# Performance work log

Measured on AMD Instinct MI355X. Metric: run time of the kernel, lower is better.

## Reference

```python
import jax, jax.numpy as jnp
import numpy as np

B, S, DIN = 2, 2048, 1024
H = 16
DK = 1024   # dim_key_query_all
DV = 1024   # dim_value_all
DOUT = 1024
HEAD_SIZE = DK / H  # attention_head_size (float division in source)
LN_EPS = 1e-5


def setup_inputs() -> dict:
    key = jax.random.key(0)
    ks = jax.random.split(key, 12)
    s_in = 1.0 / np.sqrt(DIN)
    s_dv = 1.0 / np.sqrt(DV)
    return {
        "hidden_states": jax.random.normal(ks[0], (B, S, DIN), jnp.float32),
        "Wq": jax.random.uniform(ks[1], (DK, DIN), jnp.float32, -s_in, s_in),
        "Wk": jax.random.uniform(ks[2], (DK, DIN), jnp.float32, -s_in, s_in),
        "Wcb": jax.random.uniform(ks[3], (H, DIN), jnp.float32, -s_in, s_in),
        "Wv": jax.random.uniform(ks[4], (DV, DIN), jnp.float32, -s_in, s_in),
        "bv": jax.random.uniform(ks[5], (DV,), jnp.float32, -s_in, s_in),
        "mixing": 0.2 * jax.random.normal(ks[6], (H, DK), jnp.float32),
        "Wd": jax.random.uniform(ks[7], (DOUT, DV), jnp.float32, -s_dv, s_dv),
        "bd": jax.random.uniform(ks[8], (DOUT,), jnp.float32, -s_dv, s_dv),
        "gamma": jnp.ones((DV,), jnp.float32),
        "beta": jnp.zeros((DV,), jnp.float32),
    }


def reference(hidden_states, Wq, Wk, Wcb, Wv, bv, mixing, Wd, bd, gamma, beta):
    x = hidden_states  # [B, S, DIN]; self-attention: from == to
    q = jnp.einsum('bsd,kd->bsk', x, Wq)  # [B,S,DK]
    k = jnp.einsum('bsd,kd->bsk', x, Wk)  # [B,S,DK]
    # scores[b,h,i,j] = sum_c q[b,i,c]*mixing[h,c]*k[b,j,c]
    scores = jnp.einsum('bic,hc,bjc->bhij', q, mixing, k)
    cb = jnp.einsum('bjd,hd->bhj', x, Wcb)  # content bias [B,H,S]
    scores = scores + cb[:, :, None, :]
    scores = scores / jnp.sqrt(jnp.asarray(HEAD_SIZE, scores.dtype))
    probs = jax.nn.softmax(scores, axis=-1)  # dropout p=0.0 -> identity
    v = jnp.einsum('bsd,vd->bsv', x, Wv) + bv  # [B,S,DV]
    v = v.reshape(B, S, H, DV // H)
    ctx = jnp.einsum('bhij,bjhv->bihv', probs, v).reshape(B, S, DV)
    out = jnp.einsum('bsv,ov->bso', ctx, Wd) + bd
    res = x + out
    mu = jnp.mean(res, axis=-1, keepdims=True)
    var = jnp.var(res, axis=-1, keepdims=True)
    out = (res - mu) * jax.lax.rsqrt(var + LN_EPS) * gamma + beta
    return (out,)
```

## Files before the change

kernel.cpp:

```cpp
#include <hip/hip_runtime.h>
#include <cstddef>
#include <cstdint>

#define B_    2
#define S_    2048
#define DIN_  1024
#define H_    16
#define DK_   1024
#define DV_   1024
#define DH_   64
#define DOUT_ 1024
#define M_    (B_ * S_)

typedef __attribute__((ext_vector_type(8)))  short short8;
typedef __attribute__((ext_vector_type(4)))  float float4v;
typedef __attribute__((ext_vector_type(16))) float float16v;
typedef _Float16 half8v __attribute__((ext_vector_type(8)));

__device__ __forceinline__ float bf16s_to_f(short s) {
  union { unsigned int u; float f; } cv;
  cv.u = ((unsigned int)(unsigned short)s) << 16;
  return cv.f;
}
__device__ __forceinline__ short f_to_bf16s(float f) {
  union { float f; unsigned int u; } cv;
  cv.f = f;
  unsigned int u = cv.u + 0x7FFFu + ((cv.u >> 16) & 1u);
  return (short)(u >> 16);
}
__device__ __forceinline__ short f_to_f16s(float f) {
  union { _Float16 h; short s; } cv;
  cv.h = (_Float16)f;
  return cv.s;
}
__device__ __forceinline__ unsigned pkrtz_u32(float a, float b) {
  union { __fp16 __attribute__((ext_vector_type(2))) h2; unsigned u; } cv;
  cv.h2 = __builtin_amdgcn_cvt_pkrtz(a, b);
  return cv.u;
}
__device__ __forceinline__ void gll16(const void* g, void* l) {
  __builtin_amdgcn_global_load_lds(
      (const __attribute__((address_space(1))) unsigned int*)g,
      (__attribute__((address_space(3))) unsigned int*)l, 16, 0, 0);
}

__global__ __launch_bounds__(256) void cast_kernel(const float* __restrict__ in,
                                                   short* __restrict__ out, int n4) {
  int i = blockIdx.x * 256 + threadIdx.x;
  if (i >= n4) return;
  float4 v = ((const float4*)in)[i];
  union { ushort4 u; short s[4]; } o;
  o.s[0] = f_to_bf16s(v.x); o.s[1] = f_to_bf16s(v.y);
  o.s[2] = f_to_bf16s(v.z); o.s[3] = f_to_bf16s(v.w);
  ((ushort4*)out)[i] = o.u;
}

__global__ __launch_bounds__(256) void cb_kernel(const float* __restrict__ x,
                                                 const float* __restrict__ Wcb,
                                                 float* __restrict__ CBs) {
  __shared__ float xs[DIN_];
  const int row = blockIdx.x;
  const int tid = threadIdx.x;
  #pragma unroll
  for (int it = 0; it < 4; ++it)
    xs[tid + it * 256] = x[(size_t)row * DIN_ + tid + it * 256];
  __syncthreads();
  const int lane = tid & 63, w = tid >> 6;
  const float SC = 0.125f * 1.44269504088896f;
  #pragma unroll
  for (int hh = 0; hh < 4; ++hh) {
    const int hidx = w * 4 + hh;
    float p = 0.f;
    for (int c = lane; c < DIN_; c += 64)
      p += xs[c] * Wcb[(size_t)hidx * DIN_ + c];
    #pragma unroll
    for (int mk = 1; mk < 64; mk <<= 1) p += __shfl_xor(p, mk);
    if (lane == 0) {
      const int bb = row / S_, ss = row % S_;
      CBs[((size_t)bb * H_ + hidx) * S_ + ss] = p * SC;
    }
  }
}

__global__ __launch_bounds__(256, 2) void gemm_qkv(
    const short* __restrict__ A, const short* __restrict__ Wqb,
    const short* __restrict__ Wkb, const short* __restrict__ Wvb,
    const float* __restrict__ bv, short* __restrict__ Qf,
    short* __restrict__ Kf, short* __restrict__ Vtf) {
  const int KD = 1024;
  __shared__ short As[64][136];
  __shared__ short Bs[64][136];
  const int tid  = threadIdx.x;
  const int lane = tid & 63;
  const int w    = tid >> 6;
  const int quad = lane >> 4;
  const int l16  = lane & 15;
  const int sel  = blockIdx.x >> 4;
  const int n0   = (blockIdx.x & 15) * 64;
  const int m0   = blockIdx.y * 64;
  const short* Bw = sel == 0 ? Wqb : (sel == 1 ? Wkb : Wvb);
  const int wm   = (w >> 1) * 32;
  const int wn   = (w & 1) * 32;
  const int srow = tid >> 2;
  const int sseg = (tid & 3) * 32;

  const float4v zero = {0.f, 0.f, 0.f, 0.f};
  float4v acc[2][2];
  acc[0][0] = zero; acc[0][1] = zero; acc[1][0] = zero; acc[1][1] = zero;

  for (int k0 = 0; k0 < KD; k0 += 128) {
    short8 ar[4], br[4];
    #pragma unroll
    for (int c = 0; c < 4; ++c) {
      ar[c] = *(const short8*)(A  + (size_t)(m0 + srow) * KD + k0 + sseg + c * 8);
      br[c] = *(const short8*)(Bw + (size_t)(n0 + srow) * KD + k0 + sseg + c * 8);
    }
    __syncthreads();
    #pragma unroll
    for (int c = 0; c < 4; ++c) {
      *(short8*)&As[srow][sseg + c * 8] = ar[c];
      *(short8*)&Bs[srow][sseg + c * 8] = br[c];
    }
    __syncthreads();
    #pragma unroll
    for (int ks = 0; ks < 4; ++ks) {
      short8 af0 = *(short8*)&As[wm + l16][ks * 32 + quad * 8];
      short8 af1 = *(short8*)&As[wm + 16 + l16][ks * 32 + quad * 8];
      short8 bg0 = *(short8*)&Bs[wn + l16][ks * 32 + quad * 8];
      short8 bg1 = *(short8*)&Bs[wn + 16 + l16][ks * 32 + quad * 8];
      acc[0][0] = __builtin_amdgcn_mfma_f32_16x16x32_bf16(af0, bg0, acc[0][0], 0, 0, 0);
      acc[0][1] = __builtin_amdgcn_mfma_f32_16x16x32_bf16(af0, bg1, acc[0][1], 0, 0, 0);
      acc[1][0] = __builtin_amdgcn_mfma_f32_16x16x32_bf16(af1, bg0, acc[1][0], 0, 0, 0);
      acc[1][1] = __builtin_amdgcn_mfma_f32_16x16x32_bf16(af1, bg1, acc[1][1], 0, 0, 0);
    }
  }

  #pragma unroll
  for (int mt = 0; mt < 2; ++mt)
    #pragma unroll
    for (int nt = 0; nt < 2; ++nt)
      #pragma unroll
      for (int r = 0; r < 4; ++r) {
        int row = m0 + wm + mt * 16 + quad * 4 + r;
        int col = n0 + wn + nt * 16 + l16;
        float v = acc[mt][nt][r];
        if (sel == 2) {
          v += bv[col];
          int bb = row >> 11, ss = row & 2047;
          Vtf[((size_t)bb * DV_ + col) * S_ + ss] = f_to_f16s(v);
        } else {
          short* o = sel == 0 ? Qf : Kf;
          o[(size_t)row * 1024 + col] = f_to_f16s(v);
        }
      }
}

__global__ __launch_bounds__(256, 2) void gemm_out(
    const short* __restrict__ A, const short* __restrict__ Bw,
    const float* __restrict__ bias, const float* __restrict__ resid,
    float* __restrict__ outf) {
  const int KD = 1024, ND = 1024;
  __shared__ short As[64][136];
  __shared__ short Bs[64][136];
  const int tid  = threadIdx.x;
  const int lane = tid & 63;
  const int w    = tid >> 6;
  const int quad = lane >> 4;
  const int l16  = lane & 15;
  const int m0   = blockIdx.y * 64;
  const int n0   = blockIdx.x * 64;
  const int wm   = (w >> 1) * 32;
  const int wn   = (w & 1) * 32;
  const int srow = tid >> 2;
  const int sseg = (tid & 3) * 32;

  const float4v zero = {0.f, 0.f, 0.f, 0.f};
  float4v acc[2][2];
  acc[0][0] = zero; acc[0][1] = zero; acc[1][0] = zero; acc[1][1] = zero;

  for (int k0 = 0; k0 < KD; k0 += 128) {
    short8 ar[4], br[4];
    #pragma unroll
    for (int c = 0; c < 4; ++c) {
      ar[c] = *(const short8*)(A  + (size_t)(m0 + srow) * KD + k0 + sseg + c * 8);
      br[c] = *(const short8*)(Bw + (size_t)(n0 + srow) * KD + k0 + sseg + c * 8);
    }
    __syncthreads();
    #pragma unroll
    for (int c = 0; c < 4; ++c) {
      *(short8*)&As[srow][sseg + c * 8] = ar[c];
      *(short8*)&Bs[srow][sseg + c * 8] = br[c];
    }
    __syncthreads();
    #pragma unroll
    for (int ks = 0; ks < 4; ++ks) {
      short8 af0 = *(short8*)&As[wm + l16][ks * 32 + quad * 8];
      short8 af1 = *(short8*)&As[wm + 16 + l16][ks * 32 + quad * 8];
      short8 bg0 = *(short8*)&Bs[wn + l16][ks * 32 + quad * 8];
      short8 bg1 = *(short8*)&Bs[wn + 16 + l16][ks * 32 + quad * 8];
      acc[0][0] = __builtin_amdgcn_mfma_f32_16x16x32_bf16(af0, bg0, acc[0][0], 0, 0, 0);
      acc[0][1] = __builtin_amdgcn_mfma_f32_16x16x32_bf16(af0, bg1, acc[0][1], 0, 0, 0);
      acc[1][0] = __builtin_amdgcn_mfma_f32_16x16x32_bf16(af1, bg0, acc[1][0], 0, 0, 0);
      acc[1][1] = __builtin_amdgcn_mfma_f32_16x16x32_bf16(af1, bg1, acc[1][1], 0, 0, 0);
    }
  }

  #pragma unroll
  for (int mt = 0; mt < 2; ++mt)
    #pragma unroll
    for (int nt = 0; nt < 2; ++nt)
      #pragma unroll
      for (int r = 0; r < 4; ++r) {
        int row = m0 + wm + mt * 16 + quad * 4 + r;
        int col = n0 + wn + nt * 16 + l16;
        outf[(size_t)row * ND + col] =
            acc[mt][nt][r] + bias[col] + resid[(size_t)row * ND + col];
      }
}

__global__ __launch_bounds__(256, 2) void attn_kernel(
    const short* __restrict__ Qf, const short* __restrict__ Kf,
    const short* __restrict__ Vtf, const float* __restrict__ mixing,
    const float* __restrict__ CBs, short* __restrict__ ctxb) {
  __shared__ __align__(16) short Kbuf[2][128 * 64];
  __shared__ __align__(16) short Vt[64][136];
  __shared__ __align__(16) short mix_s[DK_];
  __shared__ float cb_s[128];

  const int tid  = threadIdx.x;
  const int lane = tid & 63;
  const int l32  = lane & 31;
  const int l1   = lane >> 5;
  const int w    = tid >> 6;

  const int F    = blockIdx.x;
  const int xcd  = F & 7, rest = F >> 3;
  const int b    = xcd >> 2;
  const int h    = (xcd & 3) * 4 + (rest & 3);
  const int i0   = (rest >> 2) * 128;

  const float SC = 0.125f * 1.44269504088896f;
  for (int c = tid; c < DK_; c += 256) {
    union { _Float16 h; short s; } cv;
    cv.h = (_Float16)(mixing[(size_t)h * DK_ + c] * SC);
    mix_s[c] = cv.s;
  }

  const int iq = i0 + w * 32 + l32;
  const short* qptr  = Qf + ((size_t)b * S_ + iq) * DK_;
  const short* kbase = Kf + (size_t)b * S_ * DK_;
  const short* vtb   = Vtf + ((size_t)b * DV_ + h * DH_) * S_;
  const float* cbp   = CBs + ((size_t)b * H_ + h) * S_;

  float16v accS[4], accO[2];
  #pragma unroll
  for (int g = 0; g < 2; ++g)
    #pragma unroll
    for (int r = 0; r < 16; ++r) accO[g][r] = 0.f;
  float m_run = -1e30f, l_run = 0.f;

  const int dr   = lane >> 3;
  const int lch  = (lane & 7) ^ dr;
  const int axor = l32 & 7;

  const int vrow = tid >> 2;
  const int vseg = (tid & 3) * 32;

  for (int j0 = 0; j0 < S_; j0 += 128) {
    short8 vreg[4];
    #pragma unroll
    for (int c = 0; c < 4; ++c)
      vreg[c] = *(const short8*)(vtb + (size_t)vrow * S_ + j0 + vseg + c * 8);
    float cbv = 0.f;
    if (tid < 128) cbv = cbp[j0 + tid];
    __syncthreads();
    #pragma unroll
    for (int c = 0; c < 4; ++c)
      *(short8*)&Vt[vrow][vseg + c * 8] = vreg[c];
    if (tid < 128) cb_s[tid] = cbv;

    #pragma unroll
    for (int cc = 0; cc < 4; ++cc) {
      const int n = w * 4 + cc, row = 8 * n + dr;
      gll16(kbase + (size_t)(j0 + row) * DK_ + lch * 8, &Kbuf[0][n * 512]);
    }
    half8v qcur[4];
    #pragma unroll
    for (int ks = 0; ks < 4; ++ks)
      qcur[ks] = *(const half8v*)(qptr + ks * 16 + l1 * 8);

    #pragma unroll
    for (int f = 0; f < 4; ++f)
      #pragma unroll
      for (int r = 0; r < 16; ++r) accS[f][r] = 0.f;

    #pragma unroll 2
    for (int c = 0; c < 16; ++c) {
      __syncthreads();
      if (c < 15) {
        const int cs = c + 1;
        #pragma unroll
        for (int cc = 0; cc < 4; ++cc) {
          const int n = w * 4 + cc, row = 8 * n + dr;
          gll16(kbase + (size_t)(j0 + row) * DK_ + cs * 64 + lch * 8,
                &Kbuf[cs & 1][n * 512]);
        }
      }
      half8v qnext[4];
      if (c < 15) {
        #pragma unroll
        for (int ks = 0; ks < 4; ++ks)
          qnext[ks] = *(const half8v*)(qptr + (c + 1) * 64 + ks * 16 + l1 * 8);
      }
      const short* kb = &Kbuf[c & 1][0];
      #pragma unroll
      for (int ks = 0; ks < 4; ++ks) {
        half8v mf = *(half8v*)&mix_s[c * 64 + ks * 16 + l1 * 8];
        half8v qm = qcur[ks] * mf;
        #pragma unroll
        for (int f = 0; f < 4; ++f) {
          const int r = f * 32 + l32;
          half8v af = *(const half8v*)&kb[r * 64 + ((2 * ks + l1) ^ axor) * 8];
          accS[f] = __builtin_amdgcn_mfma_f32_32x32x16_f16(af, qm, accS[f], 0, 0, 0);
        }
      }
      if (c < 15) {
        #pragma unroll
        for (int ks = 0; ks < 4; ++ks) qcur[ks] = qnext[ks];
      }
    }

    float tmax = -1e30f;
    #pragma unroll
    for (int f = 0; f < 4; ++f)
      #pragma unroll
      for (int q = 0; q < 4; ++q) {
        float4 cbq = *(float4*)&cb_s[f * 32 + q * 8 + l1 * 4];
        #pragma unroll
        for (int c = 0; c < 4; ++c) {
          accS[f][4 * q + c] += ((const float*)&cbq)[c];
          tmax = fmaxf(tmax, accS[f][4 * q + c]);
        }
      }
    tmax = fmaxf(tmax, __shfl_xor(tmax, 32));
    const float mnew = fmaxf(m_run, tmax);
    const float alpha = exp2f(m_run - mnew);
    float tsum = 0.f;
    #pragma unroll
    for (int f = 0; f < 4; ++f)
      #pragma unroll
      for (int r = 0; r < 16; ++r) {
        float pv = exp2f(accS[f][r] - mnew);
        accS[f][r] = pv;
        tsum += pv;
      }
    tsum += __shfl_xor(tsum, 32);
    l_run = l_run * alpha + tsum;
    m_run = mnew;
    #pragma unroll
    for (int g = 0; g < 2; ++g)
      #pragma unroll
      for (int r = 0; r < 16; ++r) accO[g][r] *= alpha;

    #pragma unroll
    for (int cpv = 0; cpv < 8; ++cpv) {
      const int t = cpv & 1, fp = cpv >> 1;
      float xo[4], yo[4], lo[4], hi[4];
      #pragma unroll
      for (int c = 0; c < 4; ++c) {
        xo[c] = __shfl_xor(accS[fp][8 * t + c], 32);
        yo[c] = __shfl_xor(accS[fp][8 * t + 4 + c], 32);
      }
      #pragma unroll
      for (int c = 0; c < 4; ++c) {
        lo[c] = l1 ? yo[c] : accS[fp][8 * t + c];
        hi[c] = l1 ? accS[fp][8 * t + 4 + c] : xo[c];
      }
      union { half8v v; unsigned u[4]; } pb;
      pb.u[0] = pkrtz_u32(lo[0], lo[1]);
      pb.u[1] = pkrtz_u32(lo[2], lo[3]);
      pb.u[2] = pkrtz_u32(hi[0], hi[1]);
      pb.u[3] = pkrtz_u32(hi[2], hi[3]);
      #pragma unroll
      for (int g = 0; g < 2; ++g) {
        half8v vf = *(half8v*)&Vt[g * 32 + l32][cpv * 16 + l1 * 8];
        accO[g] = __builtin_amdgcn_mfma_f32_32x32x16_f16(vf, pb.v, accO[g], 0, 0, 0);
      }
    }
  }

  const float rl = 1.0f / l_run;
  short* cbase = ctxb + ((size_t)b * S_ + iq) * DV_ + h * DH_;
  #pragma unroll
  for (int g = 0; g < 2; ++g)
    #pragma unroll
    for (int q = 0; q < 4; ++q) {
      const int dv = g * 32 + 8 * q + 4 * l1;
      union { ushort4 u4; short s[4]; } ov;
      #pragma unroll
      for (int r = 0; r < 4; ++r)
        ov.s[r] = f_to_bf16s(accO[g][4 * q + r] * rl);
      *(ushort4*)(cbase + dv) = ov.u4;
    }
}

__global__ __launch_bounds__(256) void ln_kernel(float* __restrict__ out,
                                                 const float* __restrict__ gamma,
                                                 const float* __restrict__ beta) {
  __shared__ float red[8];
  const int row = blockIdx.x;
  const int tid = threadIdx.x;
  float* p = out + (size_t)row * DOUT_;
  float4 v = ((const float4*)p)[tid];
  float s = v.x + v.y + v.z + v.w;
  #pragma unroll
  for (int mk = 1; mk < 64; mk <<= 1) s += __shfl_xor(s, mk);
  if ((tid & 63) == 0) red[tid >> 6] = s;
  __syncthreads();
  const float mean = (red[0] + red[1] + red[2] + red[3]) * (1.0f / 1024.0f);
  const float d0 = v.x - mean, d1 = v.y - mean, d2 = v.z - mean, d3 = v.w - mean;
  float sq = d0 * d0 + d1 * d1 + d2 * d2 + d3 * d3;
  #pragma unroll
  for (int mk = 1; mk < 64; mk <<= 1) sq += __shfl_xor(sq, mk);
  if ((tid & 63) == 0) red[4 + (tid >> 6)] = sq;
  __syncthreads();
  const float var = (red[4] + red[5] + red[6] + red[7]) * (1.0f / 1024.0f);
  const float rstd = rsqrtf(var + 1e-5f);
  float4 g = ((const float4*)gamma)[tid];
  float4 bt = ((const float4*)beta)[tid];
  float4 o;
  o.x = d0 * rstd * g.x + bt.x;
  o.y = d1 * rstd * g.y + bt.y;
  o.z = d2 * rstd * g.z + bt.z;
  o.w = d3 * rstd * g.w + bt.w;
  ((float4*)p)[tid] = o;
}

extern "C" void kernel_launch(void* const* d_in, const int* in_sizes, int n_in,
                              void* d_out, int out_size, void* d_ws, size_t ws_size,
                              hipStream_t stream) {
  (void)in_sizes; (void)n_in; (void)out_size; (void)ws_size;
  const float* x      = (const float*)d_in[0];
  const float* Wq     = (const float*)d_in[1];
  const float* Wk     = (const float*)d_in[2];
  const float* Wcb    = (const float*)d_in[3];
  const float* Wv     = (const float*)d_in[4];
  const float* bv     = (const float*)d_in[5];
  const float* mixing = (const float*)d_in[6];
  const float* Wd     = (const float*)d_in[7];
  const float* bd     = (const float*)d_in[8];
  const float* gamma  = (const float*)d_in[9];
  const float* beta   = (const float*)d_in[10];
  float* out = (float*)d_out;

  short* p = (short*)d_ws;
  short* xb   = p; p += (size_t)M_ * DIN_;
  short* Qf   = p; p += (size_t)M_ * DK_;
  short* Kf   = p; p += (size_t)M_ * DK_;
  short* Vtf  = p; p += (size_t)B_ * DV_ * S_;
  short* ctxb = p; p += (size_t)M_ * DV_;
  short* Wqb  = p; p += (size_t)DK_ * DIN_;
  short* Wkb  = p; p += (size_t)DK_ * DIN_;
  short* Wvb  = p; p += (size_t)DV_ * DIN_;
  short* Wdb  = p; p += (size_t)DOUT_ * DV_;
  float* CBs  = (float*)p;

  cast_kernel<<<dim3(M_ * DIN_ / 1024), 256, 0, stream>>>(x, xb, M_ * DIN_ / 4);
  cast_kernel<<<dim3(DK_ * DIN_ / 1024), 256, 0, stream>>>(Wq, Wqb, DK_ * DIN_ / 4);
  cast_kernel<<<dim3(DK_ * DIN_ / 1024), 256, 0, stream>>>(Wk, Wkb, DK_ * DIN_ / 4);
  cast_kernel<<<dim3(DV_ * DIN_ / 1024), 256, 0, stream>>>(Wv, Wvb, DV_ * DIN_ / 4);
  cast_kernel<<<dim3(DOUT_ * DV_ / 1024), 256, 0, stream>>>(Wd, Wdb, DOUT_ * DV_ / 4);
  cb_kernel<<<dim3(M_), 256, 0, stream>>>(x, Wcb, CBs);

  gemm_qkv<<<dim3(48, M_ / 64), 256, 0, stream>>>(xb, Wqb, Wkb, Wvb, bv, Qf, Kf, Vtf);

  attn_kernel<<<dim3(512), 256, 0, stream>>>(Qf, Kf, Vtf, mixing, CBs, ctxb);

  gemm_out<<<dim3(16, M_ / 64), 256, 0, stream>>>(ctxb, Wdb, bd, x, out);
  ln_kernel<<<dim3(M_), 256, 0, stream>>>(out, gamma, beta);
}
```

Before: 661.5 us.

## Widen K chunks and stream V/content-bias through shared double buffer in attention

The attention kernel now loads K in 128-wide column chunks, giving 8 chunks per key tile instead of 16, so it needs half as many barriers. V and the content bias are loaded asynchronously with global_load_lds into the same double buffer and overlap the last K chunk. The next tile's first K chunk is issued during softmax and PV. This replaces the synchronous register-staged V copy and the separate Vt and cb_s buffers, and uses an XOR swizzle over 16 columns. Shared memory rises to about 66KB, which may limit occupancy at two blocks per CU, and holding 16 Q registers raises register pressure.

```diff
diff --git a/kernel.cpp b/kernel.cpp
--- a/kernel.cpp
+++ b/kernel.cpp
@@ -42,6 +42,11 @@
   __builtin_amdgcn_global_load_lds(
       (const __attribute__((address_space(1))) unsigned int*)g,
       (__attribute__((address_space(3))) unsigned int*)l, 16, 0, 0);
+}
+__device__ __forceinline__ void gll4(const void* g, void* l) {
+  __builtin_amdgcn_global_load_lds(
+      (const __attribute__((address_space(1))) unsigned int*)g,
+      (__attribute__((address_space(3))) unsigned int*)l, 4, 0, 0);
 }
 
 __global__ __launch_bounds__(256) void cast_kernel(const float* __restrict__ in,
@@ -222,10 +227,8 @@
     const short* __restrict__ Qf, const short* __restrict__ Kf,
     const short* __restrict__ Vtf, const float* __restrict__ mixing,
     const float* __restrict__ CBs, short* __restrict__ ctxb) {
-  __shared__ __align__(16) short Kbuf[2][128 * 64];
-  __shared__ __align__(16) short Vt[64][136];
+  __shared__ __align__(16) short Kbuf[2][128 * 128];
   __shared__ __align__(16) short mix_s[DK_];
-  __shared__ float cb_s[128];
 
   const int tid  = threadIdx.x;
   const int lane = tid & 63;
@@ -252,6 +255,38 @@
   const short* vtb   = Vtf + ((size_t)b * DV_ + h * DH_) * S_;
   const float* cbp   = CBs + ((size_t)b * H_ + h) * S_;
 
+  const int drow = lane >> 4;
+  const int dp   = lane & 15;
+
+  auto issueK = [&](int j0, int kc, int bsel) {
+    short* dst = &Kbuf[bsel][0];
+    #pragma unroll
+    for (int cc = 0; cc < 8; ++cc) {
+      const int n = w * 8 + cc;
+      const int row = 4 * n + drow;
+      const int L = dp ^ (row & 15);
+      gll16(kbase + (size_t)(j0 + row) * DK_ + kc * 128 + L * 8, dst + n * 512);
+    }
+  };
+  auto issueV = [&](int j0, int bsel) {
+    short* dst = &Kbuf[bsel][0];
+    #pragma unroll
+    for (int cc = 0; cc < 4; ++cc) {
+      const int n = w * 4 + cc;
+      const int row = 4 * n + drow;
+      const int L = dp ^ (row & 15);
+      gll16(vtb + (size_t)row * S_ + j0 + L * 8, dst + n * 512);
+    }
+    float* cbl = (float*)&Kbuf[bsel][8192];
+    if (w == 0)      gll4(cbp + j0 + lane, cbl);
+    else if (w == 1) gll4(cbp + j0 + 64 + lane, cbl + 64);
+  };
+  auto loadQ = [&](int kc, half8v* q) {
+    #pragma unroll
+    for (int ks = 0; ks < 8; ++ks)
+      q[ks] = *(const half8v*)(qptr + kc * 128 + ks * 16 + l1 * 8);
+  };
+
   float16v accS[4], accO[2];
   #pragma unroll
   for (int g = 0; g < 2; ++g)
@@ -259,83 +294,56 @@
     for (int r = 0; r < 16; ++r) accO[g][r] = 0.f;
   float m_run = -1e30f, l_run = 0.f;
 
-  const int dr   = lane >> 3;
-  const int lch  = (lane & 7) ^ dr;
-  const int axor = l32 & 7;
-
-  const int vrow = tid >> 2;
-  const int vseg = (tid & 3) * 32;
-
-  for (int j0 = 0; j0 < S_; j0 += 128) {
-    short8 vreg[4];
-    #pragma unroll
-    for (int c = 0; c < 4; ++c)
-      vreg[c] = *(const short8*)(vtb + (size_t)vrow * S_ + j0 + vseg + c * 8);
-    float cbv = 0.f;
-    if (tid < 128) cbv = cbp[j0 + tid];
-    __syncthreads();
-    #pragma unroll
-    for (int c = 0; c < 4; ++c)
-      *(short8*)&Vt[vrow][vseg + c * 8] = vreg[c];
-    if (tid < 128) cb_s[tid] = cbv;
-
-    #pragma unroll
-    for (int cc = 0; cc < 4; ++cc) {
-      const int n = w * 4 + cc, row = 8 * n + dr;
-      gll16(kbase + (size_t)(j0 + row) * DK_ + lch * 8, &Kbuf[0][n * 512]);
-    }
-    half8v qcur[4];
-    #pragma unroll
-    for (int ks = 0; ks < 4; ++ks)
-      qcur[ks] = *(const half8v*)(qptr + ks * 16 + l1 * 8);
-
+  issueK(0, 0, 0);
+  half8v qcur[8], qnext[8];
+  loadQ(0, qcur);
+
+  int cur = 0;
+  for (int t = 0; t < 16; ++t) {
+    const int j0 = t * 128;
     #pragma unroll
     for (int f = 0; f < 4; ++f)
       #pragma unroll
       for (int r = 0; r < 16; ++r) accS[f][r] = 0.f;
 
-    #pragma unroll 2
-    for (int c = 0; c < 16; ++c) {
+    #pragma unroll
+    for (int kc = 0; kc < 8; ++kc) {
       __syncthreads();
-      if (c < 15) {
-        const int cs = c + 1;
-        #pragma unroll
-        for (int cc = 0; cc < 4; ++cc) {
-          const int n = w * 4 + cc, row = 8 * n + dr;
-          gll16(kbase + (size_t)(j0 + row) * DK_ + cs * 64 + lch * 8,
-                &Kbuf[cs & 1][n * 512]);
-        }
-      }
-      half8v qnext[4];
-      if (c < 15) {
-        #pragma unroll
-        for (int ks = 0; ks < 4; ++ks)
-          qnext[ks] = *(const half8v*)(qptr + (c + 1) * 64 + ks * 16 + l1 * 8);
-      }
-      const short* kb = &Kbuf[c & 1][0];
-      #pragma unroll
-      for (int ks = 0; ks < 4; ++ks) {
-        half8v mf = *(half8v*)&mix_s[c * 64 + ks * 16 + l1 * 8];
+      if (kc < 7) {
+        issueK(j0, kc + 1, cur ^ 1);
+        loadQ(kc + 1, qnext);
+      } else {
+        issueV(j0, cur ^ 1);
+        if (t < 15) loadQ(0, qnext);
+      }
+      const short* kb = &Kbuf[cur][0];
+      #pragma unroll
+      for (int ks = 0; ks < 8; ++ks) {
+        half8v mf = *(half8v*)&mix_s[kc * 128 + ks * 16 + l1 * 8];
         half8v qm = qcur[ks] * mf;
         #pragma unroll
         for (int f = 0; f < 4; ++f) {
-          const int r = f * 32 + l32;
-          half8v af = *(const half8v*)&kb[r * 64 + ((2 * ks + l1) ^ axor) * 8];
+          const int R = f * 32 + l32;
+          const int phys = (2 * ks + l1) ^ (l32 & 15);
+          half8v af = *(const half8v*)&kb[R * 128 + phys * 8];
           accS[f] = __builtin_amdgcn_mfma_f32_32x32x16_f16(af, qm, accS[f], 0, 0, 0);
         }
       }
-      if (c < 15) {
-        #pragma unroll
-        for (int ks = 0; ks < 4; ++ks) qcur[ks] = qnext[ks];
-      }
-    }
+      #pragma unroll
+      for (int ks = 0; ks < 8; ++ks) qcur[ks] = qnext[ks];
+      cur ^= 1;
+    }
+
+    __syncthreads();
+    if (t < 15) issueK(j0 + 128, 0, cur ^ 1);
+    const float* cbf = (const float*)&Kbuf[cur][8192];
 
     float tmax = -1e30f;
     #pragma unroll
     for (int f = 0; f < 4; ++f)
       #pragma unroll
       for (int q = 0; q < 4; ++q) {
-        float4 cbq = *(float4*)&cb_s[f * 32 + q * 8 + l1 * 4];
+        float4 cbq = *(float4*)&cbf[f * 32 + q * 8 + l1 * 4];
         #pragma unroll
         for (int c = 0; c < 4; ++c) {
           accS[f][4 * q + c] += ((const float*)&cbq)[c];
@@ -364,17 +372,17 @@
 
     #pragma unroll
     for (int cpv = 0; cpv < 8; ++cpv) {
-      const int t = cpv & 1, fp = cpv >> 1;
+      const int tt = cpv & 1, fp = cpv >> 1;
       float xo[4], yo[4], lo[4], hi[4];
       #pragma unroll
       for (int c = 0; c < 4; ++c) {
-        xo[c] = __shfl_xor(accS[fp][8 * t + c], 32);
-        yo[c] = __shfl_xor(accS[fp][8 * t + 4 + c], 32);
+        xo[c] = __shfl_xor(accS[fp][8 * tt + c], 32);
+        yo[c] = __shfl_xor(accS[fp][8 * tt + 4 + c], 32);
       }
       #pragma unroll
       for (int c = 0; c < 4; ++c) {
-        lo[c] = l1 ? yo[c] : accS[fp][8 * t + c];
-        hi[c] = l1 ? accS[fp][8 * t + 4 + c] : xo[c];
+        lo[c] = l1 ? yo[c] : accS[fp][8 * tt + c];
+        hi[c] = l1 ? accS[fp][8 * tt + 4 + c] : xo[c];
       }
       union { half8v v; unsigned u[4]; } pb;
       pb.u[0] = pkrtz_u32(lo[0], lo[1]);
@@ -383,10 +391,13 @@
       pb.u[3] = pkrtz_u32(hi[2], hi[3]);
       #pragma unroll
       for (int g = 0; g < 2; ++g) {
-        half8v vf = *(half8v*)&Vt[g * 32 + l32][cpv * 16 + l1 * 8];
+        const int R = g * 32 + l32;
+        const int phys = (2 * cpv + l1) ^ (l32 & 15);
+        half8v vf = *(const half8v*)&Kbuf[cur][R * 128 + phys * 8];
         accO[g] = __builtin_amdgcn_mfma_f32_32x32x16_f16(vf, pb.v, accO[g], 0, 0, 0);
       }
     }
+    cur ^= 1;
   }
 
   const float rl = 1.0f / l_run;
```

Measured after the change: 814.6 us. 23.1% more time.
